# Kernel tuning notes

Measured on AMD Instinct MI355X. Metric: run time of the kernel, lower is better.

The kernel has to match this reference:

```python
import jax, jax.numpy as jnp
import numpy as np

B = 2
SEQ_LEN = 192
DIM = 384
HEADS = 8
DIM_HEAD = 48
INNER = HEADS * DIM_HEAD  # 384
EPS = 1e-5


def setup_inputs() -> dict:
    key = jax.random.key(0)
    kx, kq, kk, kv, ko, kb = jax.random.split(key, 6)
    s = 1.0 / np.sqrt(DIM)
    return {
        "x": jax.random.normal(kx, (B, SEQ_LEN, DIM), dtype=jnp.float32),
        "gamma": jnp.ones((DIM,), jnp.float32),
        "beta": jnp.zeros((DIM,), jnp.float32),
        "u_q": jax.random.uniform(kq, (SEQ_LEN, DIM, INNER), jnp.float32, -s, s),
        "u_k": jax.random.uniform(kk, (SEQ_LEN, DIM, INNER), jnp.float32, -s, s),
        "w_v": jax.random.uniform(kv, (DIM, INNER), jnp.float32, -s, s),
        "w_o": jax.random.uniform(ko, (INNER, DIM), jnp.float32, -1.0 / np.sqrt(INNER), 1.0 / np.sqrt(INNER)),
        "b_o": jax.random.uniform(kb, (DIM,), jnp.float32, -1.0 / np.sqrt(INNER), 1.0 / np.sqrt(INNER)),
    }


def reference(x, gamma, beta, u_q, u_k, w_v, w_o, b_o):
    b, L, _ = x.shape
    h, dh = HEADS, DIM_HEAD
    scale = dh ** -0.5

    # LayerNorm (biased variance, like torch)
    mu = x.mean(-1, keepdims=True)
    var = x.var(-1, keepdims=True)
    xn = (x - mu) / jnp.sqrt(var + EPS) * gamma + beta

    # v: [b, h, n, dh]
    v = jnp.einsum('bnd,de->bne', xn, w_v).reshape(b, L, h, dh).transpose(0, 2, 1, 3)

    # Per-offset projections (avoids torch's [L,L,dim,inner] gathered weight):
    # q_all[b,i,r,:] = xn[b,i] @ u_q[r];  k_all[b,j,r,:] = xn[b,j] @ u_k[r]
    q_all = jnp.einsum('bid,rde->bire', xn, u_q)  # [b, L, L, inner]
    k_all = jnp.einsum('bjd,rde->bjre', xn, u_k)  # [b, L, L, inner]

    i = jnp.arange(L)[:, None]
    j = jnp.arange(L)[None, :]
    r = jnp.maximum(i - j, 0)  # max(0, i-j): index map of CausalSharedParameter
    ii = jnp.broadcast_to(i, (L, L))
    jj = jnp.broadcast_to(j, (L, L))

    # Torch: q[b,h,i,j] uses Wq[j,i] = u_q[min(0,j-i)+L-1] = u_q[L-1-r]
    #        k[b,h,i,j] uses Wk[i,j] = u_k[max(0,i-j)]     = u_k[r]
    q_g = q_all[:, ii, (L - 1) - r, :].reshape(b, L, L, h, dh)
    k_g = k_all[:, jj, r, :].reshape(b, L, L, h, dh)

    dots = jnp.einsum('bijhd,bijhd->bhij', q_g, k_g) * scale
    dots = jnp.where(i >= j, dots, -jnp.inf)  # causal mask
    attn = jax.nn.softmax(dots, axis=-1)

    out = jnp.einsum('bhij,bhjd->bhid', attn, v)
    out = out.transpose(0, 2, 1, 3).reshape(b, L, h * dh)
    return out @ w_o + b_o
```

## Files before the change

kernel.cpp:

```cpp
#include <hip/hip_runtime.h>

#define SEQ 192
#define DIMK 384
#define NHEAD 8
#define DHEAD 48
#define NB 2
#define SOFF (64 * 49)

typedef __attribute__((ext_vector_type(8))) short short8;
typedef __attribute__((ext_vector_type(4))) float f32x4;
typedef __attribute__((ext_vector_type(4))) unsigned int u32x4;

__device__ __forceinline__ unsigned short f2bf(float f) {
    unsigned int u = __builtin_bit_cast(unsigned int, f);
    u += 0x7FFFu + ((u >> 16) & 1u);
    return (unsigned short)(u >> 16);
}
__device__ __forceinline__ unsigned pack2(float a, float b) {
    return (unsigned)f2bf(a) | ((unsigned)f2bf(b) << 16);
}

__global__ __launch_bounds__(64) void ln_kernel(const float* __restrict__ x,
                                                const float* __restrict__ gamma,
                                                const float* __restrict__ beta,
                                                unsigned short* __restrict__ xn) {
    int row = blockIdx.x;
    int l = threadIdx.x;
    const float* xr = x + (size_t)row * DIMK;
    float v[6];
    float s = 0.f, s2 = 0.f;
#pragma unroll
    for (int k = 0; k < 6; ++k) {
        v[k] = xr[l + 64 * k];
        s += v[k];
        s2 += v[k] * v[k];
    }
#pragma unroll
    for (int off = 32; off > 0; off >>= 1) {
        s += __shfl_xor(s, off, 64);
        s2 += __shfl_xor(s2, off, 64);
    }
    float mu = s * (1.f / 384.f);
    float var = s2 * (1.f / 384.f) - mu * mu;
    float inv = rsqrtf(var + 1e-5f);
#pragma unroll
    for (int k = 0; k < 6; ++k) {
        int c = l + 64 * k;
        float o = (v[k] - mu) * inv * gamma[c] + beta[c];
        xn[(size_t)row * DIMK + c] = f2bf(o);
    }
}

__device__ __forceinline__ void gemm192(const unsigned short* __restrict__ A,
                                        const float* __restrict__ W,
                                        const float* __restrict__ bias,
                                        float* __restrict__ outp,
                                        int rowg, int colg, float* lds_f, int tid) {
    const int wave = tid >> 6, lane = tid & 63, quad = lane >> 4, l15 = lane & 15;
    const int nbase = colg * 48;
    const float* gp[3];
    int la[3];
#pragma unroll
    for (int it = 0; it < 3; ++it) {
        int idx = tid + 256 * it;
        int r = idx / 12, n0 = (idx % 12) * 4;
        gp[it] = W + (size_t)r * DIMK + nbase + n0;
        la[it] = r * 49 + n0;
    }
    const unsigned short* aptr[3];
#pragma unroll
    for (int p = 0; p < 3; ++p) {
        int row = rowg * 192 + wave * 48 + p * 16 + l15;
        aptr[p] = A + (size_t)row * DIMK + quad * 8;
    }
    f32x4 acc[3][3];
#pragma unroll
    for (int p = 0; p < 3; ++p)
#pragma unroll
        for (int nt = 0; nt < 3; ++nt) acc[p][nt] = f32x4{0.f, 0.f, 0.f, 0.f};
    f32x4 cur[3];
#pragma unroll
    for (int it = 0; it < 3; ++it) cur[it] = *(const f32x4*)gp[it];
    for (int c = 0; c < 6; ++c) {
#pragma unroll
        for (int it = 0; it < 3; ++it) {
            float* d = lds_f + la[it];
            d[0] = cur[it].x;
            d[1] = cur[it].y;
            d[2] = cur[it].z;
            d[3] = cur[it].w;
        }
        __syncthreads();
        if (c < 5) {
#pragma unroll
            for (int it = 0; it < 3; ++it)
                cur[it] = *(const f32x4*)(gp[it] + (size_t)(c + 1) * 64 * DIMK);
        }
        short8 afr[6];
#pragma unroll
        for (int p = 0; p < 3; ++p)
#pragma unroll
            for (int kk = 0; kk < 2; ++kk)
                afr[p * 2 + kk] =
                    __builtin_bit_cast(short8, *(const u32x4*)(aptr[p] + c * 64 + kk * 32));
#pragma unroll
        for (int kk = 0; kk < 2; ++kk) {
            short8 bfr[3];
#pragma unroll
            for (int nt = 0; nt < 3; ++nt) {
                const float* bsrc = lds_f + (kk * 32 + quad * 8) * 49 + nt * 16 + l15;
                u32x4 pk;
                pk.x = pack2(bsrc[0], bsrc[49]);
                pk.y = pack2(bsrc[98], bsrc[147]);
                pk.z = pack2(bsrc[196], bsrc[245]);
                pk.w = pack2(bsrc[294], bsrc[343]);
                bfr[nt] = __builtin_bit_cast(short8, pk);
            }
#pragma unroll
            for (int p = 0; p < 3; ++p)
#pragma unroll
                for (int nt = 0; nt < 3; ++nt)
                    acc[p][nt] = __builtin_amdgcn_mfma_f32_16x16x32_bf16(afr[p * 2 + kk], bfr[nt],
                                                                         acc[p][nt], 0, 0, 0);
        }
        __syncthreads();
    }
#pragma unroll
    for (int p = 0; p < 3; ++p)
#pragma unroll
        for (int nt = 0; nt < 3; ++nt) {
            int col = nbase + nt * 16 + l15;
            float badd = bias ? bias[col] : 0.f;
#pragma unroll
            for (int rr = 0; rr < 4; ++rr) {
                int row = rowg * 192 + wave * 48 + p * 16 + quad * 4 + rr;
                outp[(size_t)row * DIMK + col] = acc[p][nt][rr] + badd;
            }
        }
}

__global__ __launch_bounds__(256) void qk_kernel(const unsigned short* __restrict__ xn,
                                                 const float* __restrict__ uq,
                                                 const float* __restrict__ uk,
                                                 const float* __restrict__ wv,
                                                 float* __restrict__ dots,
                                                 float* __restrict__ vout) {
    __shared__ float lds_f[2 * SOFF];
    const int bx = blockIdx.x;
    const int tid = threadIdx.x;
    if (bx >= 2304) {
        int id = bx - 2304;
        gemm192(xn, wv, nullptr, vout, id & 1, id >> 1, lds_f, tid);
        return;
    }
    const int wave = tid >> 6, lane = tid & 63, quad = lane >> 4, l15 = lane & 15;
    const int h = bx / 288;
    int rem = bx % 288;
    int o, pass;
    if (rem < 192) {
        o = rem >> 1;
        pass = rem & 1;
    } else {
        o = rem - 96;
        pass = 0;
    }
    const int Lo = SEQ - o, Mrows = 2 * Lo;
    const int side = wave >> 1, wrow = wave & 1;
    const int rowbase = pass * 192 + wrow * 96;
    const bool active = rowbase < Mrows;
    const float* Wq = uq + (size_t)(191 - o) * (DIMK * DIMK);
    const float* Wk = uk + (size_t)o * (DIMK * DIMK);
    const int hbase = h * DHEAD;

    const float* gp[6];
    int la[6];
#pragma unroll
    for (int it = 0; it < 6; ++it) {
        int idx = tid + 256 * it;
        int m = idx / 768, r2 = idx % 768;
        int r = r2 / 12, n0 = (r2 % 12) * 4;
        gp[it] = (m ? Wk : Wq) + (size_t)r * DIMK + hbase + n0;
        la[it] = (m * 64 + r) * 49 + n0;
    }
    const unsigned short* aptr[6];
#pragma unroll
    for (int p = 0; p < 6; ++p) {
        int r = rowbase + p * 16 + l15;
        int bb = (r >= Lo) ? 1 : 0;
        int t = r - bb * Lo;
        int g = bb * SEQ + t + (side == 0 ? o : 0);
        if (r >= Mrows) g = 0;
        aptr[p] = xn + (size_t)g * DIMK + quad * 8;
    }

    f32x4 acc[6][3];
#pragma unroll
    for (int p = 0; p < 6; ++p)
#pragma unroll
        for (int nt = 0; nt < 3; ++nt) acc[p][nt] = f32x4{0.f, 0.f, 0.f, 0.f};

    f32x4 cur[6];
#pragma unroll
    for (int it = 0; it < 6; ++it) cur[it] = *(const f32x4*)gp[it];

    for (int c = 0; c < 6; ++c) {
#pragma unroll
        for (int it = 0; it < 6; ++it) {
            float* d = lds_f + la[it];
            d[0] = cur[it].x;
            d[1] = cur[it].y;
            d[2] = cur[it].z;
            d[3] = cur[it].w;
        }
        __syncthreads();
        if (c < 5) {
#pragma unroll
            for (int it = 0; it < 6; ++it)
                cur[it] = *(const f32x4*)(gp[it] + (size_t)(c + 1) * 64 * DIMK);
        }
        if (active) {
            short8 afr[12];
#pragma unroll
            for (int p = 0; p < 6; ++p)
#pragma unroll
                for (int kk = 0; kk < 2; ++kk)
                    afr[p * 2 + kk] =
                        __builtin_bit_cast(short8, *(const u32x4*)(aptr[p] + c * 64 + kk * 32));
#pragma unroll
            for (int kk = 0; kk < 2; ++kk) {
                short8 bfr[3];
#pragma unroll
                for (int nt = 0; nt < 3; ++nt) {
                    const float* bsrc =
                        lds_f + side * SOFF + (kk * 32 + quad * 8) * 49 + nt * 16 + l15;
                    u32x4 pk;
                    pk.x = pack2(bsrc[0], bsrc[49]);
                    pk.y = pack2(bsrc[98], bsrc[147]);
                    pk.z = pack2(bsrc[196], bsrc[245]);
                    pk.w = pack2(bsrc[294], bsrc[343]);
                    bfr[nt] = __builtin_bit_cast(short8, pk);
                }
#pragma unroll
                for (int p = 0; p < 6; ++p)
#pragma unroll
                    for (int nt = 0; nt < 3; ++nt)
                        acc[p][nt] = __builtin_amdgcn_mfma_f32_16x16x32_bf16(
                            afr[p * 2 + kk], bfr[nt], acc[p][nt], 0, 0, 0);
            }
        }
        __syncthreads();
    }

    float* epi = lds_f;
#pragma unroll
    for (int ph = 0; ph < 2; ++ph) {
        if (side == 1 && wrow == ph && active) {
#pragma unroll
            for (int p = 0; p < 6; ++p)
#pragma unroll
                for (int nt = 0; nt < 3; ++nt)
#pragma unroll
                    for (int r = 0; r < 4; ++r)
                        epi[((p * 3 + nt) * 4 + r) * 64 + lane] = acc[p][nt][r];
        }
        __syncthreads();
        if (side == 0 && wrow == ph && active) {
#pragma unroll
            for (int p = 0; p < 6; ++p) {
                float d0 = 0.f, d1 = 0.f, d2 = 0.f, d3 = 0.f;
#pragma unroll
                for (int nt = 0; nt < 3; ++nt) {
                    d0 += acc[p][nt][0] * epi[((p * 3 + nt) * 4 + 0) * 64 + lane];
                    d1 += acc[p][nt][1] * epi[((p * 3 + nt) * 4 + 1) * 64 + lane];
                    d2 += acc[p][nt][2] * epi[((p * 3 + nt) * 4 + 2) * 64 + lane];
                    d3 += acc[p][nt][3] * epi[((p * 3 + nt) * 4 + 3) * 64 + lane];
                }
#pragma unroll
                for (int mm = 1; mm <= 8; mm <<= 1) {
                    d0 += __shfl_xor(d0, mm, 64);
                    d1 += __shfl_xor(d1, mm, 64);
                    d2 += __shfl_xor(d2, mm, 64);
                    d3 += __shfl_xor(d3, mm, 64);
                }
                if (l15 == 0) {
                    float dv[4] = {d0, d1, d2, d3};
#pragma unroll
                    for (int r = 0; r < 4; ++r) {
                        int grow = rowbase + p * 16 + quad * 4 + r;
                        if (grow < Mrows) {
                            int bb = (grow >= Lo) ? 1 : 0;
                            int t = grow - bb * Lo;
                            int ii = t + o, jj = t;
                            dots[(((size_t)bb * NHEAD + h) * SEQ + ii) * SEQ + jj] =
                                0.14433756729740643f * dv[r];
                        }
                    }
                }
            }
        }
        __syncthreads();
    }
}

__global__ __launch_bounds__(256) void attn_kernel(const float* __restrict__ dots,
                                                   const float* __restrict__ v,
                                                   unsigned short* __restrict__ inner) {
    __shared__ float p_lds[8 * 200];
    const int i = blockIdx.x;
    const int b = blockIdx.y;
    const int tid = threadIdx.x;
    const int wave = tid >> 6, lane = tid & 63;
    const int n = i + 1;
#pragma unroll
    for (int hh = 0; hh < 2; ++hh) {
        int h = wave * 2 + hh;
        const float* drow = dots + (((size_t)b * NHEAD + h) * SEQ + i) * SEQ;
        float x0 = (lane < n) ? drow[lane] : -1e30f;
        float x1 = (lane + 64 < n) ? drow[lane + 64] : -1e30f;
        float x2 = (lane + 128 < n) ? drow[lane + 128] : -1e30f;
        float m = fmaxf(x0, fmaxf(x1, x2));
#pragma unroll
        for (int off = 32; off > 0; off >>= 1) m = fmaxf(m, __shfl_xor(m, off, 64));
        float e0 = __expf(x0 - m), e1 = __expf(x1 - m), e2 = __expf(x2 - m);
        float s = e0 + e1 + e2;
#pragma unroll
        for (int off = 32; off > 0; off >>= 1) s += __shfl_xor(s, off, 64);
        float rinv = 1.f / s;
        p_lds[h * 200 + lane] = e0 * rinv;
        p_lds[h * 200 + lane + 64] = e1 * rinv;
        p_lds[h * 200 + lane + 128] = e2 * rinv;
    }
    __syncthreads();
    const int e0 = tid;
    const int h0 = e0 / 48;
    const float* p0 = p_lds + h0 * 200;
    const int h1 = (tid < 128) ? (tid + 256) / 48 : 0;
    const float* p1 = p_lds + h1 * 200;
    const float* vb = v + (size_t)b * SEQ * DIMK;
    float a0 = 0.f, a1 = 0.f;
    const bool lo = (tid < 128);
#pragma unroll 4
    for (int j = 0; j < n; ++j) {
        a0 = fmaf(p0[j], vb[(size_t)j * DIMK + e0], a0);
        if (lo) a1 = fmaf(p1[j], vb[(size_t)j * DIMK + tid + 256], a1);
    }
    inner[((size_t)b * SEQ + i) * DIMK + e0] = f2bf(a0);
    if (lo) inner[((size_t)b * SEQ + i) * DIMK + tid + 256] = f2bf(a1);
}

__global__ __launch_bounds__(256) void proj_kernel(const unsigned short* __restrict__ inner,
                                                   const float* __restrict__ wo,
                                                   const float* __restrict__ bo,
                                                   float* __restrict__ out) {
    __shared__ float lds_f[SOFF];
    int id = blockIdx.x;
    gemm192(inner, wo, bo, out, id & 1, id >> 1, lds_f, threadIdx.x);
}

extern "C" void kernel_launch(void* const* d_in, const int* in_sizes, int n_in,
                              void* d_out, int out_size, void* d_ws, size_t ws_size,
                              hipStream_t stream) {
    const float* x = (const float*)d_in[0];
    const float* gamma = (const float*)d_in[1];
    const float* beta = (const float*)d_in[2];
    const float* uq = (const float*)d_in[3];
    const float* uk = (const float*)d_in[4];
    const float* wv = (const float*)d_in[5];
    const float* wo = (const float*)d_in[6];
    const float* bo = (const float*)d_in[7];
    float* out = (float*)d_out;

    char* ws = (char*)d_ws;
    unsigned short* xn = (unsigned short*)ws;
    float* dots = (float*)(ws + 294912);
    float* v = (float*)(ws + 294912 + 2359296);
    unsigned short* inner = (unsigned short*)(ws + 294912 + 2359296 + 589824);

    ln_kernel<<<NB * SEQ, 64, 0, stream>>>(x, gamma, beta, xn);
    qk_kernel<<<2320, 256, 0, stream>>>(xn, uq, uk, wv, dots, v);
    attn_kernel<<<dim3(SEQ, NB), 256, 0, stream>>>(dots, v, inner);
    proj_kernel<<<16, 256, 0, stream>>>(inner, wo, bo, out);
}
```

Baseline: 405.0 us.

## Stream weight tiles into double-buffered LDS with direct global-to-LDS loads

In qk_kernel, the per-thread register staging of the fp32 Wq/Wk tiles is replaced by global_load_lds DMA into two LDS buffers. The next tile is prefetched while MFMAs consume the current one, which leaves one barrier per iteration. This frees registers and VALU store work and aims for better load/compute overlap; launch bounds now request three blocks per CU. The LDS row padding (stride 49) is dropped to 48 so the 16-byte DMA layout stays contiguous, which may bring back LDS bank conflicts on the B-fragment reads.

Measured after the change: 383.7 us. 1.06x faster.

```diff
diff --git a/kernel.cpp b/kernel.cpp
--- a/kernel.cpp
+++ b/kernel.cpp
@@ -18,6 +18,10 @@
 }
 __device__ __forceinline__ unsigned pack2(float a, float b) {
     return (unsigned)f2bf(a) | ((unsigned)f2bf(b) << 16);
+}
+__device__ __forceinline__ void dma16(const float* g, void* l) {
+    __builtin_amdgcn_global_load_lds((const __attribute__((address_space(1))) void*)g,
+                                     (__attribute__((address_space(3))) void*)l, 16, 0, 0);
 }
 
 __global__ __launch_bounds__(64) void ln_kernel(const float* __restrict__ x,
@@ -139,13 +143,13 @@
         }
 }
 
-__global__ __launch_bounds__(256) void qk_kernel(const unsigned short* __restrict__ xn,
-                                                 const float* __restrict__ uq,
-                                                 const float* __restrict__ uk,
-                                                 const float* __restrict__ wv,
-                                                 float* __restrict__ dots,
-                                                 float* __restrict__ vout) {
-    __shared__ float lds_f[2 * SOFF];
+__global__ __launch_bounds__(256, 3) void qk_kernel(const unsigned short* __restrict__ xn,
+                                                    const float* __restrict__ uq,
+                                                    const float* __restrict__ uk,
+                                                    const float* __restrict__ wv,
+                                                    float* __restrict__ dots,
+                                                    float* __restrict__ vout) {
+    __shared__ __align__(16) float lds_f[2 * 6144];
     const int bx = blockIdx.x;
     const int tid = threadIdx.x;
     if (bx >= 2304) {
@@ -172,15 +176,17 @@
     const float* Wk = uk + (size_t)o * (DIMK * DIMK);
     const int hbase = h * DHEAD;
 
-    const float* gp[6];
-    int la[6];
-#pragma unroll
-    for (int it = 0; it < 6; ++it) {
-        int idx = tid + 256 * it;
-        int m = idx / 768, r2 = idx % 768;
-        int r = r2 / 12, n0 = (r2 % 12) * 4;
-        gp[it] = (m ? Wk : Wq) + (size_t)r * DIMK + hbase + n0;
-        la[it] = (m * 64 + r) * 49 + n0;
+    const float* gsrc[6];
+    unsigned ldsb[6];
+#pragma unroll
+    for (int i = 0; i < 6; ++i) {
+        int t = wave * 6 + i;
+        int u = t * 64 + lane;
+        int m = (u >= 768) ? 1 : 0;
+        int q = u - m * 768;
+        int r = q / 12, n4 = q % 12;
+        gsrc[i] = (m ? Wk : Wq) + (size_t)r * DIMK + hbase + n4 * 4;
+        ldsb[i] = (unsigned)t * 1024u;
     }
     const unsigned short* aptr[6];
 #pragma unroll
@@ -199,26 +205,19 @@
 #pragma unroll
         for (int nt = 0; nt < 3; ++nt) acc[p][nt] = f32x4{0.f, 0.f, 0.f, 0.f};
 
-    f32x4 cur[6];
-#pragma unroll
-    for (int it = 0; it < 6; ++it) cur[it] = *(const f32x4*)gp[it];
+#pragma unroll
+    for (int i = 0; i < 6; ++i) dma16(gsrc[i], (char*)lds_f + ldsb[i]);
 
     for (int c = 0; c < 6; ++c) {
-#pragma unroll
-        for (int it = 0; it < 6; ++it) {
-            float* d = lds_f + la[it];
-            d[0] = cur[it].x;
-            d[1] = cur[it].y;
-            d[2] = cur[it].z;
-            d[3] = cur[it].w;
-        }
         __syncthreads();
         if (c < 5) {
-#pragma unroll
-            for (int it = 0; it < 6; ++it)
-                cur[it] = *(const f32x4*)(gp[it] + (size_t)(c + 1) * 64 * DIMK);
+            unsigned nb = ((unsigned)(c + 1) & 1u) * 24576u;
+#pragma unroll
+            for (int i = 0; i < 6; ++i)
+                dma16(gsrc[i] + (size_t)(c + 1) * 24576, (char*)lds_f + nb + ldsb[i]);
         }
         if (active) {
+            const float* buf = lds_f + (c & 1) * 6144 + side * 3072;
             short8 afr[12];
 #pragma unroll
             for (int p = 0; p < 6; ++p)
@@ -231,13 +230,12 @@
                 short8 bfr[3];
 #pragma unroll
                 for (int nt = 0; nt < 3; ++nt) {
-                    const float* bsrc =
-                        lds_f + side * SOFF + (kk * 32 + quad * 8) * 49 + nt * 16 + l15;
+                    const float* bsrc = buf + (kk * 32 + quad * 8) * 48 + nt * 16 + l15;
                     u32x4 pk;
-                    pk.x = pack2(bsrc[0], bsrc[49]);
-                    pk.y = pack2(bsrc[98], bsrc[147]);
-                    pk.z = pack2(bsrc[196], bsrc[245]);
-                    pk.w = pack2(bsrc[294], bsrc[343]);
+                    pk.x = pack2(bsrc[0], bsrc[48]);
+                    pk.y = pack2(bsrc[96], bsrc[144]);
+                    pk.z = pack2(bsrc[192], bsrc[240]);
+                    pk.w = pack2(bsrc[288], bsrc[336]);
                     bfr[nt] = __builtin_bit_cast(short8, pk);
                 }
 #pragma unroll
@@ -248,8 +246,8 @@
                             afr[p * 2 + kk], bfr[nt], acc[p][nt], 0, 0, 0);
             }
         }
-        __syncthreads();
-    }
+    }
+    __syncthreads();
 
     float* epi = lds_f;
 #pragma unroll
```
